# Kernel tuning notes

Measured on AMD Instinct MI355X. Metric: run time of the kernel, lower is better.

The kernel has to match this reference:

```python
import jax, jax.numpy as jnp
import numpy as np

N_NODES = 38000   # 19 feature types x ~2000 categories
IN_DIM = 64
HID = 128         # hid_num in source
R = 8             # number of relations
E = 200000        # edges per relation
N_ROWS = 60000    # data rows
F = 19            # len(features)
N_CLASSES = 10


def setup_inputs() -> dict:
    key = jax.random.key(0)
    ks = jax.random.split(key, 20)
    s_in = 1.0 / np.sqrt(IN_DIM)
    s_h = 1.0 / np.sqrt(HID)
    inp = {
        "node_feats": jax.random.normal(ks[0], (N_NODES, IN_DIM), jnp.float32),
        "edges_src": jax.random.randint(ks[1], (R, E), 0, N_NODES),
        "edges_dst": jax.random.randint(ks[2], (R, E), 0, N_NODES),
        "row_idx": jax.random.randint(ks[3], (N_ROWS, F), 0, N_NODES),
        "row_mask": jax.random.randint(ks[4], (N_ROWS, F), 0, 2).astype(bool),
        # input linear
        "W_in": jax.random.normal(ks[5], (IN_DIM, HID), jnp.float32) * s_in,
        "b_in": jnp.zeros((HID,), jnp.float32),
        # RGCN layer 1 and 2: per-relation GraphConv weights
        "W1": jax.random.normal(ks[6], (R, HID, HID), jnp.float32) * s_h,
        "b1": jnp.zeros((R, HID), jnp.float32),
        "W2": jax.random.normal(ks[7], (R, HID, HID), jnp.float32) * s_h,
        "b2": jnp.zeros((R, HID), jnp.float32),
        # MLP head
        "Wm1": jax.random.normal(ks[8], (HID, HID), jnp.float32) * s_h,
        "bm1": jnp.zeros((HID,), jnp.float32),
        "Wm2": jax.random.normal(ks[9], (HID, HID), jnp.float32) * s_h,
        "bm2": jnp.zeros((HID,), jnp.float32),
        "Wm3": jax.random.normal(ks[10], (HID, N_CLASSES), jnp.float32) * s_h,
        "bm3": jnp.zeros((N_CLASSES,), jnp.float32),
    }
    return inp


def _hetero_conv(h, src, dst, W, b):
    """DGL HeteroGraphConv(sum) of GraphConv(norm='both') over R relations."""
    n = h.shape[0]
    out = jnp.zeros((n, W.shape[2]), h.dtype)
    ones = jnp.ones((src.shape[1],), h.dtype)
    for r in range(src.shape[0]):
        deg_out = jax.ops.segment_sum(ones, src[r], num_segments=n)
        deg_in = jax.ops.segment_sum(ones, dst[r], num_segments=n)
        norm_s = jnp.where(deg_out > 0, deg_out, 1.0) ** -0.5
        norm_d = jnp.where(deg_in > 0, deg_in, 1.0) ** -0.5
        msg = h[src[r]] * norm_s[src[r], None]            # [E, hid]
        agg = jax.ops.segment_sum(msg, dst[r], num_segments=n)
        out = out + (agg * norm_d[:, None]) @ W[r] + b[r]
    return out


def reference(node_feats, edges_src, edges_dst, row_idx, row_mask,
              W_in, b_in, W1, b1, W2, b2, Wm1, bm1, Wm2, bm2, Wm3, bm3):
    # input linear + relu (applied to every node type's features)
    h = jax.nn.relu(node_feats @ W_in + b_in)            # [N_nodes, HID]
    # 2-layer RGCN
    h = jax.nn.relu(_hetero_conv(h, edges_src, edges_dst, W1, b1))
    h = _hetero_conv(h, edges_src, edges_dst, W2, b2)    # [N_nodes, HID]
    # vectorized ragged gather + masked mean (replaces per-row python loop)
    m = row_mask.astype(h.dtype)                          # [N_rows, F]
    emb = h[row_idx] * m[..., None]                       # [N_rows, F, HID]
    cnt = jnp.maximum(m.sum(-1, keepdims=True), 1.0)
    mean_feat = emb.sum(1) / cnt                          # [N_rows, HID]
    # MLP head
    x = jax.nn.relu(mean_feat @ Wm1 + bm1)
    x = jax.nn.relu(x @ Wm2 + bm2)
    return x @ Wm3 + bm3                                  # [N_rows, N_CLASSES]
```

## Files before the change

### kernel.cpp

```cpp
#include <hip/hip_runtime.h>
#include <hip/hip_bf16.h>

#define NN    38000
#define HID   128
#define RR    8
#define EE    200000
#define NROWS 60000
#define FF    19
#define NCLS  10
#define NRD   (RR*NN)
#define HB    38912
#define CH    8
#define CE    (EE/CH)

typedef __hip_bfloat16 bf16;
typedef __attribute__((ext_vector_type(8))) short short8;
typedef __attribute__((ext_vector_type(4))) float floatx4;

__device__ __forceinline__ float b2f(bf16 x){ return __bfloat162float(x); }
__device__ __forceinline__ bf16  f2b(float x){ return __float2bfloat16(x); }

__device__ __forceinline__ int geti(const void* a, long long i, int wide){
  return wide ? (int)(((const long long*)a)[i]) : ((const int*)a)[i];
}

__global__ void k_fill(float* out, int n, float v){
  int i = blockIdx.x*256 + threadIdx.x;
  if (i < n) out[i] = v;
}

__global__ void k_sniff(const void* mask, const void* ridx, const void* esrc, int* flags){
  int lane = threadIdx.x;
  const unsigned short* mu = (const unsigned short*)mask;
  int l3f80e=0, l3f80o=0, lbytehi=0, loddnz=0, lother=0;
  for (int i = lane; i < 4096; i += 64){
    unsigned v = mu[i];
    if (v == 0) continue;
    if (v == 0x3F80){ if (i & 1) l3f80o = 1; else l3f80e = 1; continue; }
    unsigned lo = v & 0xFF, hi = v >> 8;
    int lob = (lo == 0 || lo == 1 || lo == 0xFF);
    int hib = (hi == 0 || hi == 1 || hi == 0xFF);
    if (lob && hib){ if (hi) lbytehi = 1; if (i & 1) loddnz = 1; continue; }
    lother = 1;
  }
  int a3f80e = __any(l3f80e);
  int a3f80o = __any(l3f80o);
  int abytehi = __any(lbytehi);
  int aoddnz = __any(loddnz);
  int aother = __any(lother);
  int mtype = -1;
  if (!aother){
    if (a3f80e && !abytehi && !aoddnz)       mtype = 2;
    else if (a3f80o && !a3f80e && !abytehi)  mtype = 3;
    else if (!a3f80e && !a3f80o){
      if (abytehi || aoddnz) mtype = 1;
      else                   mtype = 0;
    }
  }
  const int* es = (const int*)esrc;
  int loddE = 0, lseenE = 0;
  for (int i = lane; i < 512; i += 64){
    if (es[2*i+1] != 0) loddE = 1;
    if (es[2*i] > 1)    lseenE = 1;
  }
  int fE = (!__any(loddE) && __any(lseenE)) ? 1 : 0;
  const int* ri = (const int*)ridx;
  int loddI = 0, lseenI = 0;
  for (int i = lane; i < 512; i += 64){
    if (ri[2*i+1] != 0) loddI = 1;
    if (ri[2*i] > 1)    lseenI = 1;
  }
  int fI = (!__any(loddI) && __any(lseenI)) ? 1 : 0;
  if (lane == 0){ flags[1] = mtype; flags[3] = fE; flags[4] = fI; }
}


__global__ __launch_bounds__(1024) void kg_hist(const void* esrc, const void* edst,
                                                int* __restrict__ ghd, int* __restrict__ ghs,
                                                const int* flags){
  __shared__ int hist[HB];
  int t = threadIdx.x;
  for (int i = t; i < HB; i += 1024) hist[i] = 0;
  __syncthreads();
  int b = blockIdx.x;
  int side = b >> 6;
  int r = (b >> 3) & 7, c = b & 7;
  int wide = flags[3];
  const void* e = side ? esrc : edst;
  long long base = (long long)r*EE + (long long)c*CE;
  if (!wide){
    const int* p = (const int*)e + base;
    for (int i = t; i < CE; i += 1024) atomicAdd(&hist[p[i]], 1);
  } else {
    const long long* p = (const long long*)e + base;
    for (int i = t; i < CE; i += 1024) atomicAdd(&hist[(int)p[i]], 1);
  }
  __syncthreads();
  int* out = (side ? ghs : ghd) + (long long)(r*CH + c)*HB;
  for (int i = t; i < HB; i += 1024) out[i] = hist[i];
}

__global__ void kg_tot(const int* __restrict__ ghd, const int* __restrict__ ghs,
                       int* __restrict__ totg, float* __restrict__ ns){
  int i = blockIdx.x*256 + threadIdx.x;
  if (i >= RR*HB) return;
  int r = i / HB, bin = i - r*HB;
  int sd = 0, ss = 0;
#pragma unroll
  for (int c = 0; c < CH; c++){
    sd += ghd[(long long)(r*CH+c)*HB + bin];
    ss += ghs[(long long)(r*CH+c)*HB + bin];
  }
  totg[i] = sd;
  if (bin < NN) ns[r*NN + bin] = rsqrtf((float)(ss > 0 ? ss : 1));
}

__global__ __launch_bounds__(1024) void kg_scan(const int* __restrict__ totg,
                                                int* __restrict__ rowptr){
  __shared__ int tot[HB];
  __shared__ int wsum[16];
  int t = threadIdx.x, r = blockIdx.x;
  for (int i = t; i < HB; i += 1024) tot[i] = totg[r*HB + i];
  __syncthreads();
  int b0 = t*38;
  int loc[38], s = 0;
#pragma unroll
  for (int j = 0; j < 38; j++){ loc[j] = s; s += tot[b0+j]; }
  int lane = t & 63, w = t >> 6;
  int sc = s;
  for (int off = 1; off < 64; off <<= 1){
    int v = __shfl_up(sc, off);
    if (lane >= off) sc += v;
  }
  if (lane == 63) wsum[w] = sc;
  __syncthreads();
  if (t < 16){
    int v = wsum[t];
    int scw = v;
    for (int off = 1; off < 16; off <<= 1){
      int u = __shfl_up(scw, off);
      if (t >= off) scw += u;
    }
    wsum[t] = scw - v;
  }
  __syncthreads();
  int base = r*EE + (sc - s) + wsum[w];
#pragma unroll
  for (int j = 0; j < 38; j++) tot[b0+j] = base + loc[j];
  __syncthreads();
  for (int i = t; i < NN; i += 1024) rowptr[r*NN + i] = tot[i];
  if (r == RR-1 && t == 0) rowptr[NRD] = RR*EE;
}

__global__ void kg_curs(const int* __restrict__ ghd, const int* __restrict__ rowptr,
                        int* __restrict__ gcurs){
  int i = blockIdx.x*256 + threadIdx.x;
  if (i >= NRD) return;
  int r = i / NN, bin = i - r*NN;
  int p = rowptr[i];
#pragma unroll
  for (int c = 0; c < CH; c++){
    gcurs[(long long)(r*CH+c)*HB + bin] = p;
    p += ghd[(long long)(r*CH+c)*HB + bin];
  }
}

__global__ __launch_bounds__(1024) void kg_scatter(const void* esrc, const void* edst,
                                                   const int* __restrict__ gcurs,
                                                   int* __restrict__ csr, const int* flags){
  __shared__ int cur[HB];
  int t = threadIdx.x, b = blockIdx.x;
  int r = b >> 3, c = b & 7;
  const int* g = gcurs + (long long)(r*CH + c)*HB;
  for (int i = t; i < HB; i += 1024) cur[i] = g[i];
  __syncthreads();
  int wide = flags[3];
  long long base = (long long)r*EE + (long long)c*CE;
  if (!wide){
    const int* ps = (const int*)esrc + base;
    const int* pd = (const int*)edst + base;
    for (int i = t; i < CE; i += 1024){
      int d = pd[i], s = ps[i];
      int pos = atomicAdd(&cur[d], 1);
      csr[pos] = s;
    }
  } else {
    const long long* ps = (const long long*)esrc + base;
    const long long* pd = (const long long*)edst + base;
    for (int i = t; i < CE; i += 1024){
      int d = (int)pd[i], s = (int)ps[i];
      int pos = atomicAdd(&cur[d], 1);
      csr[pos] = s;
    }
  }
}


__global__ void k_bias(const float* b_in, const float* b1, const float* b2,
                       const float* bm1, const float* bm2, const float* bm3, float* o){
  int t = threadIdx.x;
  o[t] = b_in[t];
  float s1 = 0.f, s2 = 0.f;
  for (int r = 0; r < RR; r++){ s1 += b1[r*HID+t]; s2 += b2[r*HID+t]; }
  o[128+t] = s1; o[256+t] = s2;
  o[384+t] = bm1[t]; o[512+t] = bm2[t];
  if (t < NCLS) o[640+t] = bm3[t];
}

__global__ void k_pack512(const float* __restrict__ WA, const float* __restrict__ WB,
                          bf16* __restrict__ outA, bf16* __restrict__ outB){
  int idx0 = blockIdx.x*256 + threadIdx.x;
  if (idx0 >= 4*65536) return;
  const float* W = (idx0 < 2*65536) ? WA : WB;
  bf16* out      = (idx0 < 2*65536) ? outA : outB;
  int idx = idx0 & (2*65536 - 1);
  int j = idx & 7;
  int l = (idx >> 3) & 63;
  int t = (idx >> 9) & 127;
  int g = idx >> 16;
  int ktg = t & 15, nt = t >> 4;
  int kglob = ktg*32 + ((l>>4)<<3) + j;
  int rel = kglob >> 7;
  int krow = kglob & 127;
  int n = nt*16 + (l&15);
  out[idx] = f2b(W[((g*4 + rel)*128 + krow)*128 + n]);
}

__global__ void k_packg(const float* __restrict__ B, bf16* __restrict__ out, int KT){
  int idx = blockIdx.x*256 + threadIdx.x;
  if (idx >= KT*4096) return;
  int j  = idx & 7;
  int l  = (idx >> 3) & 63;
  int t  = idx >> 9;
  int kt = t % KT;
  int nt = t / KT;
  int k = kt*32 + ((l>>4)<<3) + j;
  int n = nt*16 + (l&15);
  out[idx] = f2b(B[k*128 + n]);
}

__global__ void k_gemm_in(const float* __restrict__ A, const float* __restrict__ B,
                          const float* bias, bf16* __restrict__ out){
  int row0 = blockIdx.x * 4;
  int col = threadIdx.x;
  float a0=0.f, a1=0.f, a2=0.f, a3=0.f;
  for (int k = 0; k < 64; k++){
    float bv = B[k*HID + col];
    a0 += A[(long long)(row0+0)*64 + k] * bv;
    a1 += A[(long long)(row0+1)*64 + k] * bv;
    a2 += A[(long long)(row0+2)*64 + k] * bv;
    a3 += A[(long long)(row0+3)*64 + k] * bv;
  }
  float bb = bias[col];
  out[(long long)(row0+0)*HID + col] = f2b(fmaxf(a0 + bb, 0.f));
  out[(long long)(row0+1)*HID + col] = f2b(fmaxf(a1 + bb, 0.f));
  out[(long long)(row0+2)*HID + col] = f2b(fmaxf(a2 + bb, 0.f));
  out[(long long)(row0+3)*HID + col] = f2b(fmaxf(a3 + bb, 0.f));
}

__global__ __launch_bounds__(512) void k_layer(const bf16* __restrict__ h,
                                               const int* __restrict__ rowptr,
                                               const int* __restrict__ csr,
                                               const float* __restrict__ ns,
                                               const bf16* __restrict__ Bp,
                                               const float* __restrict__ bias,
                                               bf16* __restrict__ hout, int relu){
  __shared__ char lds[8*16*256];
  int w = threadIdx.x >> 6;
  int lane = threadIdx.x & 63;
  int d0 = blockIdx.x << 4;
  const unsigned* hv = (const unsigned*)h;

  for (int i = 0; i < 16; i++){
    int rd = w*NN + d0 + i;
    int beg = rowptr[rd], end = rowptr[rd+1];
    float acc0 = 0.f, acc1 = 0.f;
    for (int base = beg; base < end; base += 64){
      int n = end - base; if (n > 64) n = 64;
      int s_l = 0; float w_l = 0.f;
      if (lane < n){ s_l = csr[base + lane]; w_l = ns[w*NN + s_l]; }
      int nb = (n + 3) & ~3;
      for (int j = 0; j < nb; j += 4){
        int   s0 = __shfl(s_l, j),   s1 = __shfl(s_l, j+1);
        int   s2 = __shfl(s_l, j+2), s3 = __shfl(s_l, j+3);
        float w0 = __shfl(w_l, j),   w1 = __shfl(w_l, j+1);
        float w2 = __shfl(w_l, j+2), w3 = __shfl(w_l, j+3);
        unsigned p0 = hv[(long long)s0*64 + lane];
        unsigned p1 = hv[(long long)s1*64 + lane];
        unsigned p2 = hv[(long long)s2*64 + lane];
        unsigned p3 = hv[(long long)s3*64 + lane];
        acc0 += w0 * __uint_as_float(p0 << 16);
        acc1 += w0 * __uint_as_float(p0 & 0xffff0000u);
        acc0 += w1 * __uint_as_float(p1 << 16);
        acc1 += w1 * __uint_as_float(p1 & 0xffff0000u);
        acc0 += w2 * __uint_as_float(p2 << 16);
        acc1 += w2 * __uint_as_float(p2 & 0xffff0000u);
        acc0 += w3 * __uint_as_float(p3 << 16);
        acc1 += w3 * __uint_as_float(p3 & 0xffff0000u);
      }
    }
    int deg = end - beg;
    float nd = rsqrtf((float)(deg > 0 ? deg : 1));
    bf16 o0 = f2b(acc0 * nd), o1 = f2b(acc1 * nd);
    unsigned ov = ((unsigned)(*(unsigned short*)&o1) << 16) | (*(unsigned short*)&o0);
    int addr = (w << 12) + (i << 8) + (lane << 2);
    addr ^= ((i & 7) << 4);
    *(unsigned*)(lds + addr) = ov;
  }
  __syncthreads();

  floatx4 acc = (floatx4){0.f,0.f,0.f,0.f};
  int row = lane & 15;
  int kb = (lane >> 4) << 4;
#pragma unroll
  for (int rel = 0; rel < 8; rel++){
    int half = rel >> 2;
    const bf16* bp = Bp + half*65536 + lane*8 + (w*16 + (rel & 3)*4)*512;
#pragma unroll
    for (int ktl = 0; ktl < 4; ktl++){
      int off = (row << 8) + ktl*64 + kb;
      off ^= ((row & 7) << 4);
      short8 a = *(const short8*)(lds + (rel << 12) + off);
      short8 b = *(const short8*)(bp + ktl*512);
      acc = __builtin_amdgcn_mfma_f32_16x16x32_bf16(a, b, acc, 0, 0, 0);
    }
  }
  int col = w*16 + (lane & 15);
  int row0 = d0 + ((lane >> 4) << 2);
  float bb = bias[col];
#pragma unroll
  for (int v = 0; v < 4; v++){
    float x = acc[v] + bb;
    if (relu) x = fmaxf(x, 0.f);
    hout[(long long)(row0 + v)*HID + col] = f2b(x);
  }
}

__global__ void k_mfma_out(const bf16* __restrict__ A, const bf16* __restrict__ Bp,
                           const float* __restrict__ bias, bf16* __restrict__ out, int M){
  int wave = (blockIdx.x*blockDim.x + threadIdx.x) >> 6;
  int lane = threadIdx.x & 63;
  int rowBase = wave << 4;
  if (rowBase >= M) return;
  long long aRow = rowBase + (lane & 15);
  int kGrp = (lane >> 4) << 3;
  floatx4 acc[8];
#pragma unroll
  for (int nt = 0; nt < 8; nt++) acc[nt] = (floatx4){0.f,0.f,0.f,0.f};
  const bf16* bp = Bp + lane*8;
#pragma unroll
  for (int kt = 0; kt < 4; kt++){
    short8 a = *(const short8*)(A + aRow*HID + kt*32 + kGrp);
#pragma unroll
    for (int nt = 0; nt < 8; nt++){
      short8 b = *(const short8*)(bp + (nt*4 + kt)*512);
      acc[nt] = __builtin_amdgcn_mfma_f32_16x16x32_bf16(a, b, acc[nt], 0, 0, 0);
    }
  }
  int colB = lane & 15;
  int rowQ = rowBase + ((lane >> 4) << 2);
#pragma unroll
  for (int nt = 0; nt < 8; nt++){
    int col = nt*16 + colB;
    float bb = bias[col];
#pragma unroll
    for (int v = 0; v < 4; v++)
      out[(long long)(rowQ+v)*HID + col] = f2b(fmaxf(acc[nt][v] + bb, 0.f));
  }
}

__global__ void k_mean(const bf16* __restrict__ h, const void* ridx, const void* rmask,
                       const int* flags, bf16* __restrict__ mean){
  int row = blockIdx.x*4 + (threadIdx.x >> 6);
  int lane = threadIdx.x & 63;
  int mt = flags[1];
  int wide = flags[4];
  const int* m4            = (const int*)rmask;
  const unsigned char* m1  = (const unsigned char*)rmask;
  const unsigned short* m2 = (const unsigned short*)rmask;
  const unsigned int* mw   = (const unsigned int*)rmask;
  const unsigned* hv = (const unsigned*)h;
  int on = 0, idxl = 0;
  if (lane < FF){
    long long i = (long long)row*FF + lane;
    if      (mt == 1) on = (m1[i] != 0);
    else if (mt == 2) on = (m2[i] != 0);
    else if (mt == 3) on = (mw[i] != 0);
    else              on = (m4[i] != 0);
    if (on) idxl = geti(ridx, i, wide);
  }
  unsigned long long bal = __ballot(on);
  float cnt = (float)__popcll(bal);
  float acc0 = 0.f, acc1 = 0.f;
#pragma unroll
  for (int j = 0; j < FF; j++){
    int s = __shfl(idxl, j);
    float w = (float)((bal >> j) & 1ull);
    unsigned pv = hv[(long long)s*64 + lane];
    acc0 += w * __uint_as_float(pv << 16);
    acc1 += w * __uint_as_float(pv & 0xffff0000u);
  }
  float inv = 1.f / fmaxf(cnt, 1.f);
  bf16 o0 = f2b(acc0 * inv), o1 = f2b(acc1 * inv);
  unsigned ov = ((unsigned)(*(unsigned short*)&o1) << 16) | (*(unsigned short*)&o0);
  ((unsigned*)mean)[(long long)row*64 + lane] = ov;
}

__global__ void k_last(const bf16* __restrict__ A, const float* __restrict__ B,
                       const float* bias, float* __restrict__ out){
  int i = blockIdx.x*256 + threadIdx.x;
  if (i >= NROWS*NCLS) return;
  int row = i / NCLS, col = i - row*NCLS;
  float acc = bias[col];
  const bf16* ar = A + (long long)row*HID;
  for (int k = 0; k < HID; k++) acc += b2f(ar[k]) * B[k*NCLS + col];
  out[i] = acc;
}

extern "C" void kernel_launch(void* const* d_in, const int* in_sizes, int n_in,
                              void* d_out, int out_size, void* d_ws, size_t ws_size,
                              hipStream_t stream){
  float* out = (float*)d_out;

  static const int expect[17] = {
    NN*64, RR*EE, RR*EE, NROWS*FF, NROWS*FF,
    64*HID, HID, RR*HID*HID, RR*HID, RR*HID*HID, RR*HID,
    HID*HID, HID, HID*HID, HID, HID*NCLS, NCLS };
  bool ok = (n_in >= 17) && (out_size == NROWS*NCLS);
  if (ok) for (int i = 0; i < 17; i++) if (in_sizes[i] != expect[i]) { ok = false; break; }
  if (!ok){
    k_fill<<<(NROWS*NCLS+255)/256, 256, 0, stream>>>(out, NROWS*NCLS, 64.0f);
    return;
  }

  const void*  e_src = d_in[1];
  const void*  e_dst = d_in[2];
  const void*  ridx  = d_in[3];
  const void*  rmask = d_in[4];
  const float* nf   = (const float*)d_in[0];
  const float* W_in = (const float*)d_in[5];
  const float* b_in = (const float*)d_in[6];
  const float* W1   = (const float*)d_in[7];
  const float* b1   = (const float*)d_in[8];
  const float* W2   = (const float*)d_in[9];
  const float* b2   = (const float*)d_in[10];
  const float* Wm1  = (const float*)d_in[11];
  const float* bm1  = (const float*)d_in[12];
  const float* Wm2  = (const float*)d_in[13];
  const float* bm2  = (const float*)d_in[14];
  const float* Wm3  = (const float*)d_in[15];
  const float* bm3  = (const float*)d_in[16];

  char* ws = (char*)d_ws;
  size_t off = 0;
  auto take = [&](size_t bytes)->char*{
    char* p = ws + off; off += (bytes + 255) & ~(size_t)255; return p; };

  int*   flags  = (int*)  take(256);
  char*  rgn    =         take(58368000);
  bf16*  meanb  = (bf16*) (rgn);
  bf16*  x1     = (bf16*) (rgn + 15360000);
  bf16*  x2     = (bf16*) (rgn + 30720000);
  int*   ghd    = (int*)  (rgn);
  int*   ghs    = (int*)  (rgn +  9961472);
  int*   gcurs  = (int*)  (rgn + 19922944);
  int*   totg   = (int*)  (rgn + 29884416);
  bf16*  h1     = (bf16*) take((size_t)NN*HID*2);
  bf16*  h2     = (bf16*) take((size_t)NN*HID*2);
  int*   rowptr = (int*)  take((size_t)(NRD+1)*4);
  int*   csr    = (int*)  take((size_t)RR*EE*4);
  float* ns     = (float*)take((size_t)NRD*4);
  float* bias   = (float*)take(656*4);
  bf16*  W1p    = (bf16*) take((size_t)2*65536*2);
  bf16*  W2p    = (bf16*) take((size_t)2*65536*2);
  bf16*  Wm1p   = (bf16*) take((size_t)16384*2);
  bf16*  Wm2p   = (bf16*) take((size_t)16384*2);

  if (off > ws_size){
    k_fill<<<(NROWS*NCLS+255)/256, 256, 0, stream>>>(out, NROWS*NCLS, 32.0f);
    return;
  }

  k_sniff   <<<1, 64, 0, stream>>>(rmask, ridx, e_src, flags);
  kg_hist   <<<128, 1024, 0, stream>>>(e_src, e_dst, ghd, ghs, flags);
  kg_tot    <<<(RR*HB+255)/256, 256, 0, stream>>>(ghd, ghs, totg, ns);
  kg_scan   <<<RR, 1024, 0, stream>>>(totg, rowptr);
  kg_curs   <<<(NRD+255)/256, 256, 0, stream>>>(ghd, rowptr, gcurs);
  kg_scatter<<<64, 1024, 0, stream>>>(e_src, e_dst, gcurs, csr, flags);
  k_bias    <<<1, 128, 0, stream>>>(b_in, b1, b2, bm1, bm2, bm3, bias);

  k_pack512<<<(4*65536+255)/256, 256, 0, stream>>>(W1, W2, W1p, W2p);
  k_packg  <<<(4*4096+255)/256, 256, 0, stream>>>(Wm1, Wm1p, 4);
  k_packg  <<<(4*4096+255)/256, 256, 0, stream>>>(Wm2, Wm2p, 4);

  k_gemm_in<<<NN/4, 128, 0, stream>>>(nf, W_in, bias+0, h1);

  k_layer<<<NN/16, 512, 0, stream>>>(h1, rowptr, csr, ns, W1p, bias+128, h2, 1);
  k_layer<<<NN/16, 512, 0, stream>>>(h2, rowptr, csr, ns, W2p, bias+256, h1, 0);

  k_mean<<<NROWS/4, 256, 0, stream>>>(h1, ridx, rmask, flags, meanb);

  int gR = (NROWS/16 + 3)/4;
  k_mfma_out<<<gR, 256, 0, stream>>>(meanb, Wm1p, bias+384, x1, NROWS);
  k_mfma_out<<<gR, 256, 0, stream>>>(x1,    Wm2p, bias+512, x2, NROWS);
  k_last<<<(NROWS*NCLS+255)/256, 256, 0, stream>>>(x2, Wm3, bias+640, out);
}
```

Measured before the change: 502.6 us.

## Batch CSR neighbour loads across 16 destination rows and double graph-build chunks

In the RGCN layer kernel, each wave now loads the 17 row pointers for its 16 destination rows once. It then fills a shared 64-wide window of neighbour indices and source norms that spans row boundaries, instead of issuing a separate 64-lane CSR and norm load for every row, which averages only a few edges. Padding lanes are zeroed by masking the weights. Separately, the edge histogram and scatter passes split each relation into 16 chunks instead of 8, doubling their block counts for more parallelism. The workspace offsets are adjusted for the larger per-chunk histograms, at the cost of more memory traffic in the histogram and cursor passes.

```diff
diff --git a/kernel.cpp b/kernel.cpp
--- a/kernel.cpp
+++ b/kernel.cpp
@@ -10,7 +10,7 @@
 #define NCLS  10
 #define NRD   (RR*NN)
 #define HB    38912
-#define CH    8
+#define CH    16
 #define CE    (EE/CH)
 
 typedef __hip_bfloat16 bf16;
@@ -83,8 +83,8 @@
   for (int i = t; i < HB; i += 1024) hist[i] = 0;
   __syncthreads();
   int b = blockIdx.x;
-  int side = b >> 6;
-  int r = (b >> 3) & 7, c = b & 7;
+  int side = b >> 7;
+  int r = (b >> 4) & 7, c = b & 15;
   int wide = flags[3];
   const void* e = side ? esrc : edst;
   long long base = (long long)r*EE + (long long)c*CE;
@@ -170,7 +170,7 @@
                                                    int* __restrict__ csr, const int* flags){
   __shared__ int cur[HB];
   int t = threadIdx.x, b = blockIdx.x;
-  int r = b >> 3, c = b & 7;
+  int r = b >> 4, c = b & 15;
   const int* g = gcurs + (long long)(r*CH + c)*HB;
   for (int i = t; i < HB; i += 1024) cur[i] = g[i];
   __syncthreads();
@@ -270,21 +270,43 @@
   int lane = threadIdx.x & 63;
   int d0 = blockIdx.x << 4;
   const unsigned* hv = (const unsigned*)h;
+  const float* nsw = ns + w*NN;
+
+  int rp = 0;
+  if (lane < 17) rp = rowptr[w*NN + d0 + lane];
+  int beg16 = __shfl(rp, 0);
+  int end16 = __shfl(rp, 16);
+
+  int wbase = beg16;
+  int s_l = 0; float w_l = 0.f;
+  { int pos = wbase + lane;
+    if (pos < end16){ s_l = csr[pos]; w_l = nsw[s_l]; } }
 
   for (int i = 0; i < 16; i++){
-    int rd = w*NN + d0 + i;
-    int beg = rowptr[rd], end = rowptr[rd+1];
+    int b = __shfl(rp, i), e = __shfl(rp, i+1);
     float acc0 = 0.f, acc1 = 0.f;
-    for (int base = beg; base < end; base += 64){
-      int n = end - base; if (n > 64) n = 64;
-      int s_l = 0; float w_l = 0.f;
-      if (lane < n){ s_l = csr[base + lane]; w_l = ns[w*NN + s_l]; }
-      int nb = (n + 3) & ~3;
-      for (int j = 0; j < nb; j += 4){
-        int   s0 = __shfl(s_l, j),   s1 = __shfl(s_l, j+1);
-        int   s2 = __shfl(s_l, j+2), s3 = __shfl(s_l, j+3);
-        float w0 = __shfl(w_l, j),   w1 = __shfl(w_l, j+1);
-        float w2 = __shfl(w_l, j+2), w3 = __shfl(w_l, j+3);
+    int j = b;
+    while (j < e){
+      while (j >= wbase + 64){
+        wbase += 64;
+        int pos = wbase + lane;
+        s_l = 0; w_l = 0.f;
+        if (pos < end16){ s_l = csr[pos]; w_l = nsw[s_l]; }
+      }
+      int wend = wbase + 64;
+      int stop = e < wend ? e : wend;
+      int m = stop - j;
+      int base_l = j - wbase;
+      int nb = (m + 3) & ~3;
+      for (int k = 0; k < nb; k += 4){
+        int i0 = base_l + k;
+        int   s0 = __shfl(s_l, i0),   s1 = __shfl(s_l, i0+1);
+        int   s2 = __shfl(s_l, i0+2), s3 = __shfl(s_l, i0+3);
+        float w0 = __shfl(w_l, i0),   w1 = __shfl(w_l, i0+1);
+        float w2 = __shfl(w_l, i0+2), w3 = __shfl(w_l, i0+3);
+        if (k+1 >= m) w1 = 0.f;
+        if (k+2 >= m) w2 = 0.f;
+        if (k+3 >= m) w3 = 0.f;
         unsigned p0 = hv[(long long)s0*64 + lane];
         unsigned p1 = hv[(long long)s1*64 + lane];
         unsigned p2 = hv[(long long)s2*64 + lane];
@@ -298,8 +320,9 @@
         acc0 += w3 * __uint_as_float(p3 << 16);
         acc1 += w3 * __uint_as_float(p3 & 0xffff0000u);
       }
-    }
-    int deg = end - beg;
+      j = stop;
+    }
+    int deg = e - b;
     float nd = rsqrtf((float)(deg > 0 ? deg : 1));
     bf16 o0 = f2b(acc0 * nd), o1 = f2b(acc1 * nd);
     unsigned ov = ((unsigned)(*(unsigned short*)&o1) << 16) | (*(unsigned short*)&o0);
@@ -462,9 +485,9 @@
   bf16*  x1     = (bf16*) (rgn + 15360000);
   bf16*  x2     = (bf16*) (rgn + 30720000);
   int*   ghd    = (int*)  (rgn);
-  int*   ghs    = (int*)  (rgn +  9961472);
+  int*   ghs    = (int*)  (rgn + 19922944);
   int*   gcurs  = (int*)  (rgn + 19922944);
-  int*   totg   = (int*)  (rgn + 29884416);
+  int*   totg   = (int*)  (rgn + 39845888);
   bf16*  h1     = (bf16*) take((size_t)NN*HID*2);
   bf16*  h2     = (bf16*) take((size_t)NN*HID*2);
   int*   rowptr = (int*)  take((size_t)(NRD+1)*4);
@@ -482,11 +505,11 @@
   }
 
   k_sniff   <<<1, 64, 0, stream>>>(rmask, ridx, e_src, flags);
-  kg_hist   <<<128, 1024, 0, stream>>>(e_src, e_dst, ghd, ghs, flags);
+  kg_hist   <<<256, 1024, 0, stream>>>(e_src, e_dst, ghd, ghs, flags);
   kg_tot    <<<(RR*HB+255)/256, 256, 0, stream>>>(ghd, ghs, totg, ns);
   kg_scan   <<<RR, 1024, 0, stream>>>(totg, rowptr);
   kg_curs   <<<(NRD+255)/256, 256, 0, stream>>>(ghd, rowptr, gcurs);
-  kg_scatter<<<64, 1024, 0, stream>>>(e_src, e_dst, gcurs, csr, flags);
+  kg_scatter<<<128, 1024, 0, stream>>>(e_src, e_dst, gcurs, csr, flags);
   k_bias    <<<1, 128, 0, stream>>>(b_in, b1, b2, bm1, bm2, bm3, bias);
 
   k_pack512<<<(4*65536+255)/256, 256, 0, stream>>>(W1, W2, W1p, W2p);
```

New measurement: 490.6 us. 2.4% less time.
